# Performance work log

Measured on AMD Instinct MI355X. Metric: run time of the kernel, lower is better.

Reference implementation:

```python
import jax, jax.numpy as jnp
import numpy as np

EPS = 1e-12

def _l2norm(x):
    # normalize rows so dot product == cosine similarity
    return x / jnp.maximum(jnp.linalg.norm(x, axis=-1, keepdims=True), EPS)

def setup_inputs() -> dict:
    key = jax.random.key(0)
    k1, k2 = jax.random.split(key)
    source_feats = jax.random.normal(k1, (4096, 1024), dtype=jnp.float32)
    target_feats = jax.random.normal(k2, (65536, 1024), dtype=jnp.float32)
    return {"source_feats": source_feats, "target_feats": target_feats, "k": 4}

def reference(source_feats, target_feats, k):
    # cosine kNN matching: for each source frame, find k nearest target frames
    # by cosine distance, then average the (raw) target features.
    sn = _l2norm(source_feats)           # [N, d]
    tn = _l2norm(target_feats)           # [M, d]
    sim = sn @ tn.T                      # [N, M] cosine similarity (dist = 1 - sim)
    _, idx = jax.lax.top_k(sim, k)       # [N, k] highest similarity == smallest cosine distance
    neighbors = target_feats[idx]        # [N, k, d] gather
    out = neighbors.mean(axis=1)         # [N, d]
    return out
```

## Files before the change

### kernel.cpp

```cpp
#include <hip/hip_runtime.h>
#include <math.h>
#include <stdint.h>

#define M     4096
#define NTGT  65536
#define KD    1024

#define NS    32
#define SLICE (NTGT / NS)
#define BT    128
#define BS    256
#define NTILE (SLICE / BT)
#define KC    32
#define TOT   (NTILE * KC)
#define NCAND 256
#define RESC  16

typedef __attribute__((ext_vector_type(4)))  int i32x4;
typedef __attribute__((ext_vector_type(16))) int i32x16;

__device__ __forceinline__ char f2i8(float x) {
    int t = __float2int_rn(x);
    t = t > 127 ? 127 : (t < -127 ? -127 : t);
    return (char)t;
}

template <int NK>
__device__ __forceinline__ void insert_desc_u(uint32_t (&arr)[NK], uint32_t pk) {
    uint32_t cur = pk;
#pragma unroll
    for (int s = 0; s < NK; ++s) {
        uint32_t old = arr[s];
        bool g = cur > old;
        arr[s] = g ? cur : old;
        cur    = g ? old : cur;
    }
}

__global__ void prep_targets(const float* __restrict__ T, float* __restrict__ tinv,
                             char* __restrict__ TqF) {
    const int wave = threadIdx.x >> 6;
    const int lane = threadIdx.x & 63;
    const int row  = blockIdx.x * 4 + wave;
    const float* p = T + (size_t)row * KD + lane * 16;
    float4 v[4];
    float s = 0.f;
#pragma unroll
    for (int j = 0; j < 4; ++j) {
        v[j] = *reinterpret_cast<const float4*>(p + j * 4);
        s += v[j].x * v[j].x + v[j].y * v[j].y + v[j].z * v[j].z + v[j].w * v[j].w;
    }
#pragma unroll
    for (int off = 32; off; off >>= 1) s += __shfl_xor(s, off);
    const float rinv = 1.0f / sqrtf(fmaxf(s, 1e-24f));
    if (lane == 0) tinv[row] = rinv;
    const float sc = rinv * 1024.0f;
    unsigned char ob[16];
#pragma unroll
    for (int j = 0; j < 4; ++j) {
        ob[j * 4 + 0] = (unsigned char)f2i8(v[j].x * sc);
        ob[j * 4 + 1] = (unsigned char)f2i8(v[j].y * sc);
        ob[j * 4 + 2] = (unsigned char)f2i8(v[j].z * sc);
        ob[j * 4 + 3] = (unsigned char)f2i8(v[j].w * sc);
    }
    const int g = row >> 5, kc = lane >> 1, h = lane & 1;
    char* dst = TqF + (size_t)g * 32768 + (size_t)(kc * 64 + (row & 31) + 32 * h) * 16;
    *reinterpret_cast<uint4*>(dst) = *reinterpret_cast<const uint4*>(ob);
}

__global__ void prep_source(const float* __restrict__ S, char* __restrict__ SqF) {
    const int wave = threadIdx.x >> 6;
    const int lane = threadIdx.x & 63;
    const int row  = blockIdx.x * 4 + wave;
    const float* p = S + (size_t)row * KD + lane * 16;
    unsigned char ob[16];
#pragma unroll
    for (int j = 0; j < 4; ++j) {
        const float4 v = *reinterpret_cast<const float4*>(p + j * 4);
        ob[j * 4 + 0] = (unsigned char)f2i8(v.x * 32.0f);
        ob[j * 4 + 1] = (unsigned char)f2i8(v.y * 32.0f);
        ob[j * 4 + 2] = (unsigned char)f2i8(v.z * 32.0f);
        ob[j * 4 + 3] = (unsigned char)f2i8(v.w * 32.0f);
    }
    const int g = row >> 5, kc = lane >> 1, h = lane & 1;
    char* dst = SqF + (size_t)g * 32768 + (size_t)(kc * 64 + (row & 31) + 32 * h) * 16;
    *reinterpret_cast<uint4*>(dst) = *reinterpret_cast<const uint4*>(ob);
}

__global__ __launch_bounds__(256, 2)
void screen_kernel(const char* __restrict__ SqF, const char* __restrict__ TqF,
                   uint32_t* __restrict__ cand_out) {
    const int tid  = threadIdx.x;
    const int lane = tid & 63, wc = tid >> 6;
    const int l31 = lane & 31, l5 = lane >> 5;
    const int bx = blockIdx.x;
    const int by = blockIdx.y;
    const int sb   = bx * BS;
    const int tgt0 = by * SLICE;

    const char* pa = TqF + (size_t)(tgt0 >> 5) * 32768 + lane * 16;
    const char* pb = SqF + (size_t)((sb >> 5) + wc * 2) * 32768 + lane * 16;

#define LOADF(A, B, gs_) do {                                                  \
        const int tt_ = (gs_) >> 5, kc_ = (gs_) & 31;                          \
        const size_t ao_ = (size_t)tt_ * 131072 + (size_t)kc_ * 1024;          \
        const size_t bo_ = (size_t)kc_ * 1024;                                 \
        A[0] = *reinterpret_cast<const i32x4*>(pa + ao_);                      \
        A[1] = *reinterpret_cast<const i32x4*>(pa + ao_ + 32768);              \
        A[2] = *reinterpret_cast<const i32x4*>(pa + ao_ + 65536);              \
        A[3] = *reinterpret_cast<const i32x4*>(pa + ao_ + 98304);              \
        B[0] = *reinterpret_cast<const i32x4*>(pb + bo_);                      \
        B[1] = *reinterpret_cast<const i32x4*>(pb + bo_ + 32768);              \
    } while (0)

#define MFMA8(A, B) do {                                                       \
        _Pragma("unroll")                                                      \
        for (int m = 0; m < 4; ++m)                                            \
            _Pragma("unroll")                                                  \
            for (int nt = 0; nt < 2; ++nt)                                     \
                acc[m][nt] = __builtin_amdgcn_mfma_i32_32x32x32_i8(            \
                    A[m], B[nt], acc[m][nt], 0, 0, 0);                         \
    } while (0)

    uint32_t cand[2][8];
#pragma unroll
    for (int nt = 0; nt < 2; ++nt)
#pragma unroll
        for (int j = 0; j < 8; ++j) cand[nt][j] = 0u;

    i32x4 aE[4], bE[2], aO[4], bO[2];
    LOADF(aE, bE, 0);

#pragma unroll 1
    for (int tt = 0; tt < NTILE; ++tt) {
        i32x16 acc[4][2];
#pragma unroll
        for (int m = 0; m < 4; ++m)
#pragma unroll
            for (int nt = 0; nt < 2; ++nt)
                acc[m][nt] = (i32x16){0,0,0,0, 0,0,0,0, 0,0,0,0, 0,0,0,0};

#pragma unroll 1
        for (int kcp = 0; kcp < KC / 2; ++kcp) {
            const int gs = tt * KC + kcp * 2;
            LOADF(aO, bO, gs + 1);
            MFMA8(aE, bE);
            if (gs + 2 < TOT) LOADF(aE, bE, gs + 2);
            MFMA8(aO, bO);
        }

        const int tb = tgt0 + tt * BT;
#pragma unroll
        for (int nt = 0; nt < 2; ++nt) {
            uint32_t c7 = cand[nt][7];
#pragma unroll
            for (int m = 0; m < 4; ++m) {
#pragma unroll
                for (int r = 0; r < 16; ++r) {
                    const int sc = acc[m][nt][r];
                    int k = (sc + (1 << 20)) >> 5;
                    k = k < 0 ? 0 : (k > 65535 ? 65535 : k);
                    const int tg = tb + m * 32 + (r & 3) + 8 * (r >> 2) + 4 * l5;
                    const uint32_t pk = ((uint32_t)k << 16) | (uint32_t)(tg & 0xFFFF);
                    if (pk > c7) {
                        insert_desc_u<8>(cand[nt], pk);
                        c7 = cand[nt][7];
                    }
                }
            }
        }
    }
#undef LOADF
#undef MFMA8

#pragma unroll
    for (int nt = 0; nt < 2; ++nt) {
        uint32_t inc[8];
#pragma unroll
        for (int j = 0; j < 8; ++j)
            inc[j] = (uint32_t)__shfl_down((int)cand[nt][j], 32);
        if (lane < 32) {
#pragma unroll
            for (int j = 0; j < 8; ++j)
                if (inc[j] > cand[nt][7]) insert_desc_u<8>(cand[nt], inc[j]);
        }
    }

    if (lane < 32) {
#pragma unroll
        for (int nt = 0; nt < 2; ++nt) {
            const int src = sb + wc * 64 + nt * 32 + l31;
            uint32_t* dst = cand_out + (size_t)src * NCAND + by * 8;
            *reinterpret_cast<uint4*>(dst)     = make_uint4(cand[nt][0], cand[nt][1], cand[nt][2], cand[nt][3]);
            *reinterpret_cast<uint4*>(dst + 4) = make_uint4(cand[nt][4], cand[nt][5], cand[nt][6], cand[nt][7]);
        }
    }
}

__global__ __launch_bounds__(256)
void final_kernel(const uint32_t* __restrict__ cand_out, const float* __restrict__ S,
                  const float* __restrict__ T, const float* __restrict__ tinv,
                  float* __restrict__ out) {
    __shared__ __align__(16) float srow[KD];
    __shared__ float rv[RESC];
    __shared__ int   ri[RESC];
    __shared__ int   sel[4];

    const int r = blockIdx.x;
    const int tid = threadIdx.x;

    *reinterpret_cast<float4*>(srow + tid * 4) =
        *reinterpret_cast<const float4*>(S + (size_t)r * KD + tid * 4);

    if (tid < 64) {
        const uint4 cv = *reinterpret_cast<const uint4*>(cand_out + (size_t)r * NCAND + tid * 4);
        uint32_t c0 = cv.x, c1 = cv.y, c2 = cv.z, c3 = cv.w;
#pragma unroll 1
        for (int it = 0; it < RESC; ++it) {
            uint32_t m01 = c0 > c1 ? c0 : c1;
            uint32_t m23 = c2 > c3 ? c2 : c3;
            uint32_t m = m01 > m23 ? m01 : m23;
#pragma unroll
            for (int off = 32; off; off >>= 1) {
                const uint32_t o = (uint32_t)__shfl_xor((int)m, off);
                m = m > o ? m : o;
            }
            if (tid == 0) ri[it] = (int)(m & 0xFFFFu);
            if      (c0 == m) c0 = 0u;
            else if (c1 == m) c1 = 0u;
            else if (c2 == m) c2 = 0u;
            else if (c3 == m) c3 = 0u;
        }
    }
    __syncthreads();

    const int lane = tid & 63, wv = tid >> 6;
    for (int c = wv; c < RESC; c += 4) {
        const int idx = ri[c];
        const float* tp = T + (size_t)idx * KD;
        float s = 0.f;
#pragma unroll
        for (int j = 0; j < 4; ++j) {
            const float4 tv = *reinterpret_cast<const float4*>(tp + lane * 4 + j * 256);
            const float4 sv = *reinterpret_cast<const float4*>(srow + lane * 4 + j * 256);
            s += tv.x * sv.x + tv.y * sv.y + tv.z * sv.z + tv.w * sv.w;
        }
#pragma unroll
        for (int off = 32; off; off >>= 1) s += __shfl_xor(s, off);
        if (lane == 0) rv[c] = s * tinv[idx];
    }
    __syncthreads();

    if (tid == 0) {
        float b0 = -INFINITY, b1 = -INFINITY, b2 = -INFINITY, b3 = -INFINITY;
        int s0 = 0, s1 = 0, s2 = 0, s3 = 0;
        for (int c = 0; c < RESC; ++c) {
            const float v = rv[c]; const int id = ri[c];
            if (v > b3) {
                if (v > b0)      { b3=b2;s3=s2; b2=b1;s2=s1; b1=b0;s1=s0; b0=v;s0=id; }
                else if (v > b1) { b3=b2;s3=s2; b2=b1;s2=s1; b1=v;s1=id; }
                else if (v > b2) { b3=b2;s3=s2; b2=v;s2=id; }
                else             { b3=v;s3=id; }
            }
        }
        sel[0]=s0; sel[1]=s1; sel[2]=s2; sel[3]=s3;
    }
    __syncthreads();

    float4 a = make_float4(0.f, 0.f, 0.f, 0.f);
#pragma unroll
    for (int q = 0; q < 4; ++q) {
        const float4 v = *reinterpret_cast<const float4*>(T + (size_t)sel[q] * KD + tid * 4);
        a.x += v.x; a.y += v.y; a.z += v.z; a.w += v.w;
    }
    a.x *= 0.25f; a.y *= 0.25f; a.z *= 0.25f; a.w *= 0.25f;
    *reinterpret_cast<float4*>(out + (size_t)r * KD + tid * 4) = a;
}

#define FNS    32
#define FSLICE (NTGT / FNS)
#define FBM 128
#define FBN 128
#define FBK 16
#define FNTILE (FSLICE / FBN)
#define FLDA 132
#define FLDSS 33

__global__ void tinv_kernel(const float* __restrict__ T, float* __restrict__ tinv) {
    const int wave = threadIdx.x >> 6;
    const int lane = threadIdx.x & 63;
    const int row  = blockIdx.x * 4 + wave;
    const float* p = T + (size_t)row * KD;
    float s = 0.f;
#pragma unroll
    for (int j = 0; j < 4; ++j) {
        float4 v = *reinterpret_cast<const float4*>(p + lane * 4 + j * 256);
        s += v.x * v.x + v.y * v.y + v.z * v.z + v.w * v.w;
    }
#pragma unroll
    for (int off = 32; off; off >>= 1) s += __shfl_xor(s, off);
    if (lane == 0) tinv[row] = 1.0f / sqrtf(fmaxf(s, 1e-24f));
}

__global__ __launch_bounds__(256, 2)
void simtopk_kernel(const float* __restrict__ S, const float* __restrict__ T,
                    const float* __restrict__ tinv,
                    float* __restrict__ pval, int* __restrict__ pidx) {
    __shared__ float smem[2 * FBK * FLDA];
    __shared__ float tinvS[FBN];
    float* As = smem;
    float* Bs = smem + FBK * FLDA;
    float* Ss = smem;

    const int tid = threadIdx.x;
    const int tx = tid & 15, ty = tid >> 4;
    const int rb   = blockIdx.x;
    const int tgt0 = blockIdx.y * FSLICE;
    const size_t abase = (size_t)(rb * FBM) * KD;

    float t0 = -INFINITY, t1 = -INFINITY, t2 = -INFINITY, t3 = -INFINITY;
    int   i0 = 0, i1 = 0, i2 = 0, i3 = 0;

    for (int nt = 0; nt < FNTILE; ++nt) {
        const int tb = tgt0 + nt * FBN;
        float acc[8][8];
#pragma unroll
        for (int i = 0; i < 8; ++i)
#pragma unroll
            for (int j = 0; j < 8; ++j) acc[i][j] = 0.f;

        for (int kk = 0; kk < KD; kk += FBK) {
            const int rr = tid >> 2;
            const int c4 = (tid & 3) * 4;
#pragma unroll
            for (int h = 0; h < 2; ++h) {
                const int row = rr + h * 64;
                float4 av = *reinterpret_cast<const float4*>(S + abase + (size_t)row * KD + kk + c4);
                float4 bv = *reinterpret_cast<const float4*>(T + (size_t)(tb + row) * KD + kk + c4);
                As[(c4 + 0) * FLDA + row] = av.x; As[(c4 + 1) * FLDA + row] = av.y;
                As[(c4 + 2) * FLDA + row] = av.z; As[(c4 + 3) * FLDA + row] = av.w;
                Bs[(c4 + 0) * FLDA + row] = bv.x; Bs[(c4 + 1) * FLDA + row] = bv.y;
                Bs[(c4 + 2) * FLDA + row] = bv.z; Bs[(c4 + 3) * FLDA + row] = bv.w;
            }
            __syncthreads();
#pragma unroll
            for (int k = 0; k < FBK; ++k) {
                float a[8], b[8];
                *reinterpret_cast<float4*>(&a[0]) = *reinterpret_cast<float4*>(&As[k * FLDA + ty * 8]);
                *reinterpret_cast<float4*>(&a[4]) = *reinterpret_cast<float4*>(&As[k * FLDA + ty * 8 + 4]);
                *reinterpret_cast<float4*>(&b[0]) = *reinterpret_cast<float4*>(&Bs[k * FLDA + tx * 4]);
                *reinterpret_cast<float4*>(&b[4]) = *reinterpret_cast<float4*>(&Bs[k * FLDA + 64 + tx * 4]);
#pragma unroll
                for (int i = 0; i < 8; ++i)
#pragma unroll
                    for (int j = 0; j < 8; ++j)
                        acc[i][j] = fmaf(a[i], b[j], acc[i][j]);
            }
            __syncthreads();
        }

        if (tid < FBN) tinvS[tid] = tinv[tb + tid];
        __syncthreads();

#pragma unroll
        for (int cc = 0; cc < 4; ++cc) {
            const int g = cc >> 1;
            if ((tx >> 3) == (cc & 1)) {
                const int txl = tx & 7;
#pragma unroll
                for (int i = 0; i < 8; ++i) {
                    const int rrow = ty * 8 + i;
#pragma unroll
                    for (int j = 0; j < 4; ++j) {
                        const int colc = 4 * txl + j;
                        Ss[rrow * FLDSS + colc] = acc[i][g * 4 + j] * tinvS[cc * 32 + colc];
                    }
                }
            }
            __syncthreads();
            if (tid < FBM) {
#pragma unroll 4
                for (int c = 0; c < 32; ++c) {
                    const float v = Ss[tid * FLDSS + c];
                    if (v > t3) {
                        const int gi = tb + cc * 32 + c;
                        if (v > t0)      { t3=t2;i3=i2; t2=t1;i2=i1; t1=t0;i1=i0; t0=v;i0=gi; }
                        else if (v > t1) { t3=t2;i3=i2; t2=t1;i2=i1; t1=v;i1=gi; }
                        else if (v > t2) { t3=t2;i3=i2; t2=v;i2=gi; }
                        else             { t3=v;i3=gi; }
                    }
                }
            }
            __syncthreads();
        }
    }

    if (tid < FBM) {
        const int row = rb * FBM + tid;
        const size_t base = ((size_t)blockIdx.y * M + row) * 4;
        pval[base + 0] = t0; pval[base + 1] = t1; pval[base + 2] = t2; pval[base + 3] = t3;
        pidx[base + 0] = i0; pidx[base + 1] = i1; pidx[base + 2] = i2; pidx[base + 3] = i3;
    }
}

__global__ void merge_kernel(const float* __restrict__ pval, const int* __restrict__ pidx,
                             const float* __restrict__ T, float* __restrict__ out) {
    __shared__ float cv[FNS * 4];
    __shared__ int   ci[FNS * 4];
    __shared__ int   sel[4];
    const int r = blockIdx.x;
    const int tid = threadIdx.x;

    if (tid < FNS * 4) {
        const int s = tid >> 2, q = tid & 3;
        const size_t base = ((size_t)s * M + r) * 4 + q;
        cv[tid] = pval[base];
        ci[tid] = pidx[base];
    }
    __syncthreads();

    if (tid == 0) {
        float t0 = -INFINITY, t1 = -INFINITY, t2 = -INFINITY, t3 = -INFINITY;
        int   j0 = 0, j1 = 0, j2 = 0, j3 = 0;
        for (int c = 0; c < FNS * 4; ++c) {
            const float v = cv[c];
            if (v > t3) {
                const int gi = ci[c];
                if (v > t0)      { t3=t2;j3=j2; t2=t1;j2=j1; t1=t0;j1=j0; t0=v;j0=gi; }
                else if (v > t1) { t3=t2;j3=j2; t2=t1;j2=j1; t1=v;j1=gi; }
                else if (v > t2) { t3=t2;j3=j2; t2=v;j2=gi; }
                else             { t3=v;j3=gi; }
            }
        }
        sel[0] = j0; sel[1] = j1; sel[2] = j2; sel[3] = j3;
    }
    __syncthreads();

    const int d = tid * 4;
    float4 a = make_float4(0.f, 0.f, 0.f, 0.f);
#pragma unroll
    for (int q = 0; q < 4; ++q) {
        const float4 v = *reinterpret_cast<const float4*>(T + (size_t)sel[q] * KD + d);
        a.x += v.x; a.y += v.y; a.z += v.z; a.w += v.w;
    }
    a.x *= 0.25f; a.y *= 0.25f; a.z *= 0.25f; a.w *= 0.25f;
    *reinterpret_cast<float4*>(out + (size_t)r * KD + d) = a;
}

extern "C" void kernel_launch(void* const* d_in, const int* in_sizes, int n_in,
                              void* d_out, int out_size, void* d_ws, size_t ws_size,
                              hipStream_t stream) {
    const float* S = (const float*)d_in[0];
    const float* T = (const float*)d_in[1];
    float* out = (float*)d_out;

    const size_t sz_tinv = (size_t)NTGT * 4;
    const size_t sz_Sq   = (size_t)M * KD;
    const size_t sz_Tq   = (size_t)NTGT * KD;
    const size_t sz_cand = (size_t)M * NCAND * 4;
    const size_t need = sz_tinv + sz_Sq + sz_Tq + sz_cand;

    if (ws_size >= need) {
        float*    tinv = (float*)d_ws;
        char*     SqF  = (char*)d_ws + sz_tinv;
        char*     TqF  = (char*)d_ws + sz_tinv + sz_Sq;
        uint32_t* cand = (uint32_t*)((char*)d_ws + sz_tinv + sz_Sq + sz_Tq);

        prep_targets<<<NTGT / 4, 256, 0, stream>>>(T, tinv, TqF);
        prep_source<<<M / 4, 256, 0, stream>>>(S, SqF);
        screen_kernel<<<dim3(M / BS, NS), 256, 0, stream>>>(SqF, TqF, cand);
        final_kernel<<<M, 256, 0, stream>>>(cand, S, T, tinv, out);
    } else {
        float* tinv = (float*)d_ws;
        float* pval = tinv + NTGT;
        int*   pidx = (int*)(pval + (size_t)FNS * M * 4);

        tinv_kernel<<<NTGT / 4, 256, 0, stream>>>(T, tinv);
        simtopk_kernel<<<dim3(M / FBM, FNS), 256, 0, stream>>>(S, T, tinv, pval, pidx);
        merge_kernel<<<M, 256, 0, stream>>>(pval, pidx, T, out);
    }
}
```

Measured before the change: 485.2 us.

## Halve screen tile height, double target slices, add raw-score threshold gating

The screen kernel now uses 64-row target tiles instead of 128, so each wave holds half the accumulators. The target dimension is split into 64 slices, so the final kernel merges 512 candidates per source row using 8 per lane. Occupancy is raised to 3 blocks per SIMD, MFMA groups are wrapped in s_setprio, and a raw integer threshold skips packing scores that cannot enter the top-8. This trades less register pressure and cheaper selection for more A-tile loads per MFMA, a per-tile __syncthreads, and twice the candidate traffic in the final kernel.

Measured after the change: 610.0 us. 1.26x slower.

```diff
diff --git a/kernel.cpp b/kernel.cpp
--- a/kernel.cpp
+++ b/kernel.cpp
@@ -6,14 +6,14 @@
 #define NTGT  65536
 #define KD    1024
 
-#define NS    32
+#define NS    64
 #define SLICE (NTGT / NS)
-#define BT    128
+#define BT    64
 #define BS    256
 #define NTILE (SLICE / BT)
 #define KC    32
 #define TOT   (NTILE * KC)
-#define NCAND 256
+#define NCAND 512
 #define RESC  16
 
 typedef __attribute__((ext_vector_type(4)))  int i32x4;
@@ -87,7 +87,7 @@
     *reinterpret_cast<uint4*>(dst) = *reinterpret_cast<const uint4*>(ob);
 }
 
-__global__ __launch_bounds__(256, 2)
+__global__ __launch_bounds__(256, 3)
 void screen_kernel(const char* __restrict__ SqF, const char* __restrict__ TqF,
                    uint32_t* __restrict__ cand_out) {
     const int tid  = threadIdx.x;
@@ -103,96 +103,99 @@
 
 #define LOADF(A, B, gs_) do {                                                  \
         const int tt_ = (gs_) >> 5, kc_ = (gs_) & 31;                          \
-        const size_t ao_ = (size_t)tt_ * 131072 + (size_t)kc_ * 1024;          \
+        const size_t ao_ = (size_t)tt_ * 65536 + (size_t)kc_ * 1024;           \
         const size_t bo_ = (size_t)kc_ * 1024;                                 \
         A[0] = *reinterpret_cast<const i32x4*>(pa + ao_);                      \
         A[1] = *reinterpret_cast<const i32x4*>(pa + ao_ + 32768);              \
-        A[2] = *reinterpret_cast<const i32x4*>(pa + ao_ + 65536);              \
-        A[3] = *reinterpret_cast<const i32x4*>(pa + ao_ + 98304);              \
         B[0] = *reinterpret_cast<const i32x4*>(pb + bo_);                      \
         B[1] = *reinterpret_cast<const i32x4*>(pb + bo_ + 32768);              \
     } while (0)
 
-#define MFMA8(A, B) do {                                                       \
+#define MFMA4(A, B) do {                                                       \
+        __builtin_amdgcn_s_setprio(1);                                         \
         _Pragma("unroll")                                                      \
-        for (int m = 0; m < 4; ++m)                                            \
+        for (int m = 0; m < 2; ++m)                                            \
             _Pragma("unroll")                                                  \
-            for (int nt = 0; nt < 2; ++nt)                                     \
-                acc[m][nt] = __builtin_amdgcn_mfma_i32_32x32x32_i8(            \
-                    A[m], B[nt], acc[m][nt], 0, 0, 0);                         \
+            for (int g = 0; g < 2; ++g)                                        \
+                acc[m][g] = __builtin_amdgcn_mfma_i32_32x32x32_i8(             \
+                    A[m], B[g], acc[m][g], 0, 0, 0);                           \
+        __builtin_amdgcn_s_setprio(0);                                         \
     } while (0)
 
     uint32_t cand[2][8];
 #pragma unroll
-    for (int nt = 0; nt < 2; ++nt)
-#pragma unroll
-        for (int j = 0; j < 8; ++j) cand[nt][j] = 0u;
-
-    i32x4 aE[4], bE[2], aO[4], bO[2];
+    for (int g = 0; g < 2; ++g)
+#pragma unroll
+        for (int j = 0; j < 8; ++j) cand[g][j] = 0u;
+    int rawthr[2] = {-(1 << 20), -(1 << 20)};
+
+    i32x4 aE[2], bE[2], aO[2], bO[2];
     LOADF(aE, bE, 0);
 
 #pragma unroll 1
     for (int tt = 0; tt < NTILE; ++tt) {
-        i32x16 acc[4][2];
-#pragma unroll
-        for (int m = 0; m < 4; ++m)
-#pragma unroll
-            for (int nt = 0; nt < 2; ++nt)
-                acc[m][nt] = (i32x16){0,0,0,0, 0,0,0,0, 0,0,0,0, 0,0,0,0};
+        i32x16 acc[2][2];
+#pragma unroll
+        for (int m = 0; m < 2; ++m)
+#pragma unroll
+            for (int g = 0; g < 2; ++g)
+                acc[m][g] = (i32x16){0,0,0,0, 0,0,0,0, 0,0,0,0, 0,0,0,0};
 
 #pragma unroll 1
         for (int kcp = 0; kcp < KC / 2; ++kcp) {
             const int gs = tt * KC + kcp * 2;
             LOADF(aO, bO, gs + 1);
-            MFMA8(aE, bE);
+            MFMA4(aE, bE);
             if (gs + 2 < TOT) LOADF(aE, bE, gs + 2);
-            MFMA8(aO, bO);
+            MFMA4(aO, bO);
         }
 
         const int tb = tgt0 + tt * BT;
 #pragma unroll
-        for (int nt = 0; nt < 2; ++nt) {
-            uint32_t c7 = cand[nt][7];
-#pragma unroll
-            for (int m = 0; m < 4; ++m) {
+        for (int g = 0; g < 2; ++g) {
+#pragma unroll
+            for (int m = 0; m < 2; ++m) {
 #pragma unroll
                 for (int r = 0; r < 16; ++r) {
-                    const int sc = acc[m][nt][r];
-                    int k = (sc + (1 << 20)) >> 5;
-                    k = k < 0 ? 0 : (k > 65535 ? 65535 : k);
-                    const int tg = tb + m * 32 + (r & 3) + 8 * (r >> 2) + 4 * l5;
-                    const uint32_t pk = ((uint32_t)k << 16) | (uint32_t)(tg & 0xFFFF);
-                    if (pk > c7) {
-                        insert_desc_u<8>(cand[nt], pk);
-                        c7 = cand[nt][7];
+                    const int sc = acc[m][g][r];
+                    if (sc >= rawthr[g]) {
+                        int k = (sc + (1 << 20)) >> 5;
+                        k = k < 0 ? 0 : (k > 65535 ? 65535 : k);
+                        const int tg = tb + m * 32 + (r & 3) + 8 * (r >> 2) + 4 * l5;
+                        const uint32_t pk = ((uint32_t)k << 16) | (uint32_t)(tg & 0xFFFF);
+                        if (pk > cand[g][7]) {
+                            insert_desc_u<8>(cand[g], pk);
+                            rawthr[g] = (((int)(cand[g][7] >> 16)) << 5) - (1 << 20);
+                        }
                     }
                 }
             }
         }
+        __syncthreads();
     }
 #undef LOADF
-#undef MFMA8
-
-#pragma unroll
-    for (int nt = 0; nt < 2; ++nt) {
+#undef MFMA4
+
+#pragma unroll
+    for (int g = 0; g < 2; ++g) {
         uint32_t inc[8];
 #pragma unroll
         for (int j = 0; j < 8; ++j)
-            inc[j] = (uint32_t)__shfl_down((int)cand[nt][j], 32);
+            inc[j] = (uint32_t)__shfl_down((int)cand[g][j], 32);
         if (lane < 32) {
 #pragma unroll
             for (int j = 0; j < 8; ++j)
-                if (inc[j] > cand[nt][7]) insert_desc_u<8>(cand[nt], inc[j]);
+                if (inc[j] > cand[g][7]) insert_desc_u<8>(cand[g], inc[j]);
         }
     }
 
     if (lane < 32) {
 #pragma unroll
-        for (int nt = 0; nt < 2; ++nt) {
-            const int src = sb + wc * 64 + nt * 32 + l31;
+        for (int g = 0; g < 2; ++g) {
+            const int src = sb + wc * 64 + g * 32 + l31;
             uint32_t* dst = cand_out + (size_t)src * NCAND + by * 8;
-            *reinterpret_cast<uint4*>(dst)     = make_uint4(cand[nt][0], cand[nt][1], cand[nt][2], cand[nt][3]);
-            *reinterpret_cast<uint4*>(dst + 4) = make_uint4(cand[nt][4], cand[nt][5], cand[nt][6], cand[nt][7]);
+            *reinterpret_cast<uint4*>(dst)     = make_uint4(cand[g][0], cand[g][1], cand[g][2], cand[g][3]);
+            *reinterpret_cast<uint4*>(dst + 4) = make_uint4(cand[g][4], cand[g][5], cand[g][6], cand[g][7]);
         }
     }
 }
@@ -213,23 +216,27 @@
         *reinterpret_cast<const float4*>(S + (size_t)r * KD + tid * 4);
 
     if (tid < 64) {
-        const uint4 cv = *reinterpret_cast<const uint4*>(cand_out + (size_t)r * NCAND + tid * 4);
-        uint32_t c0 = cv.x, c1 = cv.y, c2 = cv.z, c3 = cv.w;
+        const uint4 cv0 = *reinterpret_cast<const uint4*>(cand_out + (size_t)r * NCAND + tid * 8);
+        const uint4 cv1 = *reinterpret_cast<const uint4*>(cand_out + (size_t)r * NCAND + tid * 8 + 4);
+        uint32_t c[8] = {cv0.x, cv0.y, cv0.z, cv0.w, cv1.x, cv1.y, cv1.z, cv1.w};
 #pragma unroll 1
         for (int it = 0; it < RESC; ++it) {
-            uint32_t m01 = c0 > c1 ? c0 : c1;
-            uint32_t m23 = c2 > c3 ? c2 : c3;
-            uint32_t m = m01 > m23 ? m01 : m23;
+            uint32_t m01 = c[0] > c[1] ? c[0] : c[1];
+            uint32_t m23 = c[2] > c[3] ? c[2] : c[3];
+            uint32_t m45 = c[4] > c[5] ? c[4] : c[5];
+            uint32_t m67 = c[6] > c[7] ? c[6] : c[7];
+            uint32_t ma = m01 > m23 ? m01 : m23;
+            uint32_t mb = m45 > m67 ? m45 : m67;
+            uint32_t m = ma > mb ? ma : mb;
 #pragma unroll
             for (int off = 32; off; off >>= 1) {
                 const uint32_t o = (uint32_t)__shfl_xor((int)m, off);
                 m = m > o ? m : o;
             }
             if (tid == 0) ri[it] = (int)(m & 0xFFFFu);
-            if      (c0 == m) c0 = 0u;
-            else if (c1 == m) c1 = 0u;
-            else if (c2 == m) c2 = 0u;
-            else if (c3 == m) c3 = 0u;
+#pragma unroll
+            for (int j = 0; j < 8; ++j)
+                if (c[j] == m) { c[j] = 0u; break; }
         }
     }
     __syncthreads();
```
